# Kernel optimization log

Measured on AMD Instinct MI355X. Metric: run time of the kernel, lower is better.

## Reference

```python
import jax, jax.numpy as jnp
import numpy as np

B, C, H, W = 4, 256, 64, 64
EPS = 1e-6


def setup_inputs() -> dict:
    key = jax.random.key(0)
    ks = jax.random.split(key, 6)
    x = jax.random.normal(ks[0], (B, C, H, W), jnp.float32)
    gn_w = jnp.ones((1, C, 1, 1), jnp.float32)
    gn_b = jnp.zeros((1, C, 1, 1), jnp.float32)
    s = 1.0 / np.sqrt(C)
    w0 = jax.random.normal(ks[1], (C, C), jnp.float32) * s
    w1 = jax.random.normal(ks[2], (C, C), jnp.float32) * s
    w2 = jax.random.normal(ks[3], (C, C), jnp.float32) * s
    w3 = jax.random.normal(ks[4], (C, C), jnp.float32) * s
    b0 = jnp.zeros((C,), jnp.float32)
    b1 = jnp.zeros((C,), jnp.float32)
    b2 = jnp.zeros((C,), jnp.float32)
    b3 = jnp.zeros((C,), jnp.float32)
    return {"x": x, "gn_w": gn_w, "gn_b": gn_b,
            "w0": w0, "b0": b0, "w1": w1, "b1": b1,
            "w2": w2, "b2": b2, "w3": w3, "b3": b3}


def _nin(t, Wm, bv):
    # 1x1 conv as channel matmul: (B,C,H,W) x (C,D) -> (B,D,H,W)
    return jnp.einsum('bchw,cd->bdhw', t, Wm) + bv[None, :, None, None]


def reference(x, gn_w, gn_b, w0, b0, w1, b1, w2, b2, w3, b3):
    Bb, Cc, Hh, Ww = x.shape
    G = min(Cc // 4, 32)  # GroupLayerNorm2d groups
    # per-pixel group norm: normalize over channels within each group only
    xg = x.reshape(Bb, G, Cc // G, Hh, Ww)
    mean = xg.mean(axis=2, keepdims=True)
    var = xg.var(axis=2, keepdims=True)
    hn = ((xg - mean) / jnp.sqrt(var + EPS)).reshape(Bb, Cc, Hh, Ww)
    hn = hn * gn_w + gn_b
    q = _nin(hn, w0, b0)
    k = _nin(hn, w1, b1)
    v = _nin(hn, w2, b2)
    # full (B,H,W,H,W) scores; mask is causal along W only (key col j > query col w)
    scores = jnp.einsum('bchw,bcij->bhwij', q, k) * (float(Cc) ** -0.5)
    causal = jnp.triu(jnp.ones((Ww, Ww), bool), k=1)  # (W_query, W_key)
    scores = jnp.where(causal[None, None, :, None, :], -jnp.inf, scores)
    attn = jax.nn.softmax(scores.reshape(Bb, Hh, Ww, Hh * Ww), axis=-1)
    attn = attn.reshape(Bb, Hh, Ww, Hh, Ww)
    h = jnp.einsum('bhwij,bcij->bchw', attn, v)
    return x + _nin(h, w3, b3)  # skip_rescale=False
```

## Files before the change

### kernel.cpp

```cpp
#include <hip/hip_runtime.h>
#include <math.h>

#define LOG2E 1.4426950408889634f

typedef __attribute__((ext_vector_type(8))) __bf16 bf16x8_t;
typedef __attribute__((ext_vector_type(8))) short short8_t;
typedef __attribute__((ext_vector_type(4))) short short4_t;
typedef __attribute__((ext_vector_type(4))) float f32x4;

static __device__ __forceinline__ short f2bf(float f){
    unsigned u = __builtin_bit_cast(unsigned, f);
    unsigned r = (u + 0x7fffu + ((u >> 16) & 1u)) >> 16;
    return (short)r;
}
static __device__ __forceinline__ float bf2f(short s){
    return __builtin_bit_cast(float, (unsigned)((unsigned short)s) << 16);
}

static __device__ __forceinline__ f32x4 mfma16(short8_t a, short8_t b, f32x4 c){
    return __builtin_amdgcn_mfma_f32_16x16x32_bf16(
        __builtin_bit_cast(bf16x8_t, a), __builtin_bit_cast(bf16x8_t, b), c, 0, 0, 0);
}

static __device__ __forceinline__ float swz16(float v){
    return __builtin_bit_cast(float,
        __builtin_amdgcn_ds_swizzle(__builtin_bit_cast(int, v), 0x401F));
}
static __device__ __forceinline__ float bperm32(int addr, float v){
    return __builtin_bit_cast(float,
        __builtin_amdgcn_ds_bpermute(addr, __builtin_bit_cast(int, v)));
}

__global__ __launch_bounds__(256) void prep_w(const float* __restrict__ w0,
    const float* __restrict__ w1, const float* __restrict__ w2,
    const float* __restrict__ w3, short* __restrict__ wT)
{
    __shared__ float T[64 * 65];
    const int mat = blockIdx.x >> 4, tile = blockIdx.x & 15;
    const int c0 = (tile >> 2) * 64, d0 = (tile & 3) * 64;
    const float* src = mat == 0 ? w0 : mat == 1 ? w1 : mat == 2 ? w2 : w3;
    const int t = threadIdx.x;
    #pragma unroll
    for (int i = 0; i < 4; i++){
        int r = (t >> 4) + i * 16, c4 = (t & 15) * 4;
        f32x4 v = *(const f32x4*)(src + (size_t)(c0 + r) * 256 + d0 + c4);
        #pragma unroll
        for (int j = 0; j < 4; j++) T[r * 65 + c4 + j] = v[j];
    }
    __syncthreads();
    int drow = t >> 2, cb = (t & 3) * 16;
    short tmp[16];
    #pragma unroll
    for (int j = 0; j < 16; j++) tmp[j] = f2bf(T[(cb + j) * 65 + drow]);
    short* dst = wT + (size_t)mat * 65536 + (size_t)(d0 + drow) * 256 + c0 + cb;
    *(short8_t*)dst = *(short8_t*)tmp;
    *(short8_t*)(dst + 8) = *(short8_t*)(tmp + 8);
}

__global__ __launch_bounds__(256) void gn_kernel(const float* __restrict__ x,
    const float* __restrict__ gnw, const float* __restrict__ gnb,
    short* __restrict__ hn)
{
    int flat = blockIdx.x * 256 + threadIdx.x;
    int n = flat & 4095, g = (flat >> 12) & 31, b = flat >> 17;
    const float* xp = x + (size_t)(b * 256 + g * 8) * 4096 + n;
    float v[8], s = 0.f, s2 = 0.f;
    #pragma unroll
    for (int k = 0; k < 8; k++){ float t = xp[(size_t)k * 4096]; v[k] = t; s += t; s2 += t * t; }
    float mean = s * 0.125f;
    float var  = s2 * 0.125f - mean * mean;
    float inv  = rsqrtf(var + 1e-6f);
    int h = n >> 6, w = n & 63, m = w * 64 + h;
    short o[8];
    #pragma unroll
    for (int k = 0; k < 8; k++)
        o[k] = f2bf((v[k] - mean) * inv * gnw[g * 8 + k] + gnb[g * 8 + k]);
    *(short8_t*)(hn + (size_t)(b * 4096 + m) * 256 + g * 8) = *(short8_t*)o;
}

__global__ __launch_bounds__(256) void qkv_gemm(const short* __restrict__ hn,
    const short* __restrict__ wT, const float* __restrict__ bq,
    const float* __restrict__ bk, const float* __restrict__ bv,
    short* __restrict__ Q, short* __restrict__ Kf, short* __restrict__ Vf)
{
    __shared__ short As[64 * 72];
    __shared__ short Bs[64 * 72];
    __shared__ float CT[64 * 65];

    const int tid = threadIdx.x;
    const int m0 = blockIdx.x * 64;
    const int by = blockIdx.y;
    const int mat = by >> 2;
    const int d0 = (by & 3) * 64;
    const short* w = wT + mat * 65536;
    const float* bias = mat == 0 ? bq : mat == 1 ? bk : bv;

    const int wv = tid >> 6, lane = tid & 63;
    const int wrow = (wv >> 1) * 32, wcol = (wv & 1) * 32;
    const int lrow = lane & 15, lq = lane >> 4;

    f32x4 acc[2][2] = {};

    for (int k0 = 0; k0 < 256; k0 += 64){
        __syncthreads();
        #pragma unroll
        for (int i = 0; i < 2; i++){
            int idx = tid + i * 256, r = idx >> 3, c = (idx & 7) * 8;
            *(short8_t*)&As[r * 72 + c] = *(const short8_t*)(hn + (size_t)(m0 + r) * 256 + k0 + c);
            *(short8_t*)&Bs[r * 72 + c] = *(const short8_t*)(w  + (size_t)(d0 + r) * 256 + k0 + c);
        }
        __syncthreads();
        #pragma unroll
        for (int kk = 0; kk < 2; kk++){
            int off = kk * 32 + lq * 8;
            short8_t a0  = *(short8_t*)&As[(wrow + lrow) * 72 + off];
            short8_t a1  = *(short8_t*)&As[(wrow + 16 + lrow) * 72 + off];
            short8_t b0v = *(short8_t*)&Bs[(wcol + lrow) * 72 + off];
            short8_t b1v = *(short8_t*)&Bs[(wcol + 16 + lrow) * 72 + off];
            acc[0][0] = mfma16(a0, b0v, acc[0][0]);
            acc[0][1] = mfma16(a0, b1v, acc[0][1]);
            acc[1][0] = mfma16(a1, b0v, acc[1][0]);
            acc[1][1] = mfma16(a1, b1v, acc[1][1]);
        }
    }

    const int b = m0 >> 12, kb64 = (m0 & 4095) >> 6;

    if (mat == 0){
        #pragma unroll
        for (int i = 0; i < 2; i++)
          #pragma unroll
          for (int j = 0; j < 2; j++)
            #pragma unroll
            for (int r = 0; r < 4; r++){
                int row = wrow + i * 16 + lq * 4 + r;
                int col = wcol + j * 16 + lrow;
                Q[(size_t)(m0 + row) * 256 + d0 + col] = f2bf((acc[i][j][r] + bias[d0 + col]) * 0.0625f);
            }
    } else if (mat == 1){
        #pragma unroll
        for (int i = 0; i < 2; i++)
          #pragma unroll
          for (int j = 0; j < 2; j++)
            #pragma unroll
            for (int r = 0; r < 4; r++){
                int row = wrow + i * 16 + lq * 4 + r;
                int col = wcol + j * 16 + lrow;
                CT[row * 65 + col] = acc[i][j][r] + bias[d0 + col];
            }
        __syncthreads();
        int key = tid >> 2, c16 = (tid & 3) * 16;
        int kc = key >> 4, l15 = key & 15;
        #pragma unroll
        for (int half = 0; half < 2; half++){
            int ch0 = c16 + half * 8;
            int ks = (d0 + ch0) >> 5, lqf = (ch0 & 31) >> 3;
            short tmp[8];
            #pragma unroll
            for (int j = 0; j < 8; j++) tmp[j] = f2bf(CT[key * 65 + ch0 + j]);
            size_t base = ((((size_t)(b * 64 + kb64)) * 4 + kc) * 8 + ks) * 512 + (lqf * 16 + l15) * 8;
            *(short8_t*)(Kf + base) = *(short8_t*)tmp;
        }
    } else {
        #pragma unroll
        for (int i = 0; i < 2; i++)
          #pragma unroll
          for (int j = 0; j < 2; j++)
            #pragma unroll
            for (int r = 0; r < 4; r++){
                int row = wrow + i * 16 + lq * 4 + r;
                int col = wcol + j * 16 + lrow;
                CT[col * 65 + row] = acc[i][j][r] + bias[d0 + col];
            }
        __syncthreads();
        const int kbd = kb64 >> 1, parity = kb64 & 1;
        const int cht_l = tid >> 6, lane_s = tid & 63;
        const int l15s = lane_s & 15, lg4s = lane_s >> 4;
        const int cht = (d0 >> 4) + cht_l;
        #pragma unroll
        for (int kc = 0; kc < 4; kc++){
            short tmp[4];
            #pragma unroll
            for (int j = 0; j < 4; j++)
                tmp[j] = f2bf(CT[(cht_l * 16 + l15s) * 65 + kc * 16 + lg4s * 4 + j]);
            size_t base = (size_t)b * 1048576 + (size_t)kbd * 32768 + kc * 8192
                        + cht * 512 + lane_s * 8 + parity * 4;
            *(short4_t*)(Vf + base) = *(short4_t*)tmp;
        }
    }
}

__global__ __launch_bounds__(256, 2) void attn_kernel(const short* __restrict__ Q,
    const short* __restrict__ Kf, const short* __restrict__ Vf,
    short* __restrict__ hb)
{
    __shared__ float mls[4][16][2];
    __shared__ short LOs[4][16][264];

    const int tid = threadIdx.x, lane = tid & 63, kc = tid >> 6;
    const int l15 = lane & 15, lg4 = lane >> 4;
    const int a32 = ((lane ^ 32) << 2);

    const int id = blockIdx.x;
    const int qd = id >> 8, c = id & 255;
    const int w6 = c >> 2, hh = (c >> 1) & 1, rg = c & 1;
    const int b  = qd;
    const int w  = (qd & 1) ? 63 - w6 : w6;
    const int q0 = w * 64 + hh * 32 + rg * 16;

    const short* Kb = Kf + (size_t)b * 1048576 + kc * 4096 + lane * 8;
    const short* Vb = Vf + (size_t)b * 1048576 + kc * 8192 + lane * 8;

    short8_t qf[8];
    {
        const short* qp = Q + ((size_t)b * 4096 + q0 + l15) * 256;
        #pragma unroll
        for (int ks = 0; ks < 8; ks++)
            qf[ks] = *(const short8_t*)(qp + ks * 32 + lg4 * 8);
    }

    f32x4 oacc[16] = {};
    float m_run = -1e30f, l_run = 0.f;

    short8_t kcur[8], knext[8];
    #pragma unroll
    for (int ks = 0; ks < 8; ks++)
        kcur[ks] = *(const short8_t*)(Kb + ks * 512);

    for (int kb = 0; kb <= w; kb += 2){
        const bool has_odd = (kb + 1 <= w);
        if (has_odd){
            const short* kit = Kb + (size_t)(kb + 1) * 16384;
            #pragma unroll
            for (int ks = 0; ks < 8; ks++)
                knext[ks] = *(const short8_t*)(kit + ks * 512);
        }
        f32x4 st = {};
        #pragma unroll
        for (int ks = 0; ks < 8; ks++) st = mfma16(kcur[ks], qf[ks], st);

        if (kb + 2 <= w){
            const short* kit = Kb + (size_t)(kb + 2) * 16384;
            #pragma unroll
            for (int ks = 0; ks < 8; ks++)
                kcur[ks] = *(const short8_t*)(kit + ks * 512);
        }

        f32x4 st2 = { -1e30f, -1e30f, -1e30f, -1e30f };
        if (has_odd){
            f32x4 z = {};
            #pragma unroll
            for (int ks = 0; ks < 8; ks++) z = mfma16(knext[ks], qf[ks], z);
            st2 = z;
        }

        float tmax = fmaxf(fmaxf(fmaxf(st[0], st[1]), fmaxf(st[2], st[3])),
                           fmaxf(fmaxf(st2[0], st2[1]), fmaxf(st2[2], st2[3])));
        tmax = fmaxf(tmax, swz16(tmax));
        tmax = fmaxf(tmax, bperm32(a32, tmax));
        float m_new = fmaxf(m_run, tmax);
        float alpha = exp2f((m_run - m_new) * LOG2E);
        m_run = m_new;

        f32x4 p_e, p_o;
        #pragma unroll
        for (int r = 0; r < 4; r++){
            p_e[r] = exp2f((st[r]  - m_new) * LOG2E);
            p_o[r] = exp2f((st2[r] - m_new) * LOG2E);
        }
        float tsum = ((p_e[0] + p_e[1]) + (p_e[2] + p_e[3]))
                   + ((p_o[0] + p_o[1]) + (p_o[2] + p_o[3]));
        tsum += swz16(tsum);
        tsum += bperm32(a32, tsum);
        l_run = l_run * alpha + tsum;

        short pb[8];
        #pragma unroll
        for (int r = 0; r < 4; r++){ pb[r] = f2bf(p_e[r]); pb[4 + r] = f2bf(p_o[r]); }
        short8_t pbf = *(short8_t*)pb;

        const short* vit = Vb + (size_t)(kb >> 1) * 32768;
        #pragma unroll
        for (int cht = 0; cht < 16; cht++){
            short8_t vfr = *(const short8_t*)(vit + cht * 512);
            f32x4 t = oacc[cht];
            #pragma unroll
            for (int r = 0; r < 4; r++) t[r] *= alpha;
            oacc[cht] = mfma16(vfr, pbf, t);
        }
    }

    if (lg4 == 0){ mls[kc][l15][0] = m_run; mls[kc][l15][1] = l_run; }
    __syncthreads();
    float m0v = mls[0][l15][0], m1v = mls[1][l15][0], m2v = mls[2][l15][0], m3v = mls[3][l15][0];
    float mstar = fmaxf(fmaxf(m0v, m1v), fmaxf(m2v, m3v));
    float Lsum = mls[0][l15][1] * exp2f((m0v - mstar) * LOG2E)
               + mls[1][l15][1] * exp2f((m1v - mstar) * LOG2E)
               + mls[2][l15][1] * exp2f((m2v - mstar) * LOG2E)
               + mls[3][l15][1] * exp2f((m3v - mstar) * LOG2E);
    float sc = exp2f((m_run - mstar) * LOG2E);
    #pragma unroll
    for (int cht = 0; cht < 16; cht++){
        short t4[4];
        #pragma unroll
        for (int r = 0; r < 4; r++) t4[r] = f2bf(oacc[cht][r] * sc);
        *(short4_t*)&LOs[kc][l15][cht * 16 + lg4 * 4] = *(short4_t*)t4;
    }
    __syncthreads();
    {
        const int ch0 = kc * 64 + lg4 * 16;
        float inv = 1.f / Lsum;
        short tmp[16];
        #pragma unroll
        for (int c8 = 0; c8 < 2; c8++){
            short8_t a0 = *(const short8_t*)&LOs[0][l15][ch0 + c8 * 8];
            short8_t a1 = *(const short8_t*)&LOs[1][l15][ch0 + c8 * 8];
            short8_t a2 = *(const short8_t*)&LOs[2][l15][ch0 + c8 * 8];
            short8_t a3 = *(const short8_t*)&LOs[3][l15][ch0 + c8 * 8];
            #pragma unroll
            for (int j = 0; j < 8; j++){
                float s = (bf2f(a0[j]) + bf2f(a1[j])) + (bf2f(a2[j]) + bf2f(a3[j]));
                tmp[c8 * 8 + j] = f2bf(s * inv);
            }
        }
        const int h = hh * 32 + rg * 16 + l15;
        short* dst = hb + ((size_t)b * 4096 + h * 64 + w) * 256 + ch0;
        *(short8_t*)dst = *(short8_t*)tmp;
        *(short8_t*)(dst + 8) = *(short8_t*)(tmp + 8);
    }
}

__global__ __launch_bounds__(256) void final_gemm(const short* __restrict__ hbuf,
    const short* __restrict__ wT3, const float* __restrict__ b3,
    const float* __restrict__ x, float* __restrict__ out)
{
    __shared__ short As[64 * 72];
    __shared__ short Bs[64 * 72];
    __shared__ float CT[64 * 65];

    const int tid = threadIdx.x;
    const int m0 = blockIdx.x * 64;
    const int d0 = blockIdx.y * 64;
    const int wv = tid >> 6, lane = tid & 63;
    const int wrow = (wv >> 1) * 32, wcol = (wv & 1) * 32;
    const int lrow = lane & 15, lq = lane >> 4;

    f32x4 acc[2][2] = {};
    for (int k0 = 0; k0 < 256; k0 += 64){
        __syncthreads();
        #pragma unroll
        for (int i = 0; i < 2; i++){
            int idx = tid + i * 256, r = idx >> 3, c = (idx & 7) * 8;
            *(short8_t*)&As[r * 72 + c] = *(const short8_t*)(hbuf + (size_t)(m0 + r) * 256 + k0 + c);
            *(short8_t*)&Bs[r * 72 + c] = *(const short8_t*)(wT3 + (size_t)(d0 + r) * 256 + k0 + c);
        }
        __syncthreads();
        #pragma unroll
        for (int kk = 0; kk < 2; kk++){
            int off = kk * 32 + lq * 8;
            short8_t a0  = *(short8_t*)&As[(wrow + lrow) * 72 + off];
            short8_t a1  = *(short8_t*)&As[(wrow + 16 + lrow) * 72 + off];
            short8_t b0v = *(short8_t*)&Bs[(wcol + lrow) * 72 + off];
            short8_t b1v = *(short8_t*)&Bs[(wcol + 16 + lrow) * 72 + off];
            acc[0][0] = mfma16(a0, b0v, acc[0][0]);
            acc[0][1] = mfma16(a0, b1v, acc[0][1]);
            acc[1][0] = mfma16(a1, b0v, acc[1][0]);
            acc[1][1] = mfma16(a1, b1v, acc[1][1]);
        }
    }
    #pragma unroll
    for (int i = 0; i < 2; i++)
      #pragma unroll
      for (int j = 0; j < 2; j++)
        #pragma unroll
        for (int r = 0; r < 4; r++){
            int row = wrow + i * 16 + lq * 4 + r;
            int col = wcol + j * 16 + lrow;
            CT[col * 65 + row] = acc[i][j][r] + b3[d0 + col];
        }
    __syncthreads();
    int b = m0 >> 12, n0 = m0 & 4095, hrow = n0 >> 6;
    int dr = tid >> 2, wc = (tid & 3) * 16;
    size_t base = ((size_t)(b * 256 + d0 + dr) * 64 + hrow) * 64 + wc;
    const f32x4* xp = (const f32x4*)(x + base);
    f32x4* op = (f32x4*)(out + base);
    #pragma unroll
    for (int q = 0; q < 4; q++){
        f32x4 xv = xp[q], o;
        #pragma unroll
        for (int j = 0; j < 4; j++) o[j] = xv[j] + CT[dr * 65 + wc + q * 4 + j];
        op[q] = o;
    }
}

extern "C" void kernel_launch(void* const* d_in, const int* in_sizes, int n_in,
                              void* d_out, int out_size, void* d_ws, size_t ws_size,
                              hipStream_t stream)
{
    const float* x   = (const float*)d_in[0];
    const float* gnw = (const float*)d_in[1];
    const float* gnb = (const float*)d_in[2];
    const float* w0  = (const float*)d_in[3];
    const float* b0  = (const float*)d_in[4];
    const float* w1  = (const float*)d_in[5];
    const float* b1  = (const float*)d_in[6];
    const float* w2  = (const float*)d_in[7];
    const float* b2  = (const float*)d_in[8];
    const float* w3  = (const float*)d_in[9];
    const float* b3  = (const float*)d_in[10];
    float* out = (float*)d_out;

    char* ws = (char*)d_ws;
    short* wT  = (short*)(ws);
    short* hn  = (short*)(ws + 524288);
    short* Qb  = (short*)(ws + 8912896);
    short* Kfb = (short*)(ws + 17301504);
    short* Vfb = (short*)(ws + 25690112);
    short* hb  = (short*)(ws + 34078720);

    prep_w   <<<64, 256, 0, stream>>>(w0, w1, w2, w3, wT);
    gn_kernel<<<2048, 256, 0, stream>>>(x, gnw, gnb, hn);
    qkv_gemm <<<dim3(256, 12), 256, 0, stream>>>(hn, wT, b0, b1, b2, Qb, Kfb, Vfb);
    attn_kernel<<<1024, 256, 0, stream>>>(Qb, Kfb, Vfb, hb);
    final_gemm<<<dim3(256, 4), 256, 0, stream>>>(hb, wT + 3 * 65536, b3, x, out);
}
```

Baseline: 210.6 us.

## Fuse weight prep with groupnorm, restructure attention softmax with lazy rescale

Merges the weight-transpose and group-norm kernels into one launch to save a kernel launch. In the attention kernel it raises occupancy to 3 waves per SIMD, remaps block ids so each batch/half lands on one XCD for K/V cache locality, and uses a single K buffer. It switches to a lazy online-softmax rescale that only rescales the accumulator when the max grows by more than a threshold, and defers the row-sum reduction to the end. It also adds s_setprio around MFMA bursts and nontemporal Q loads. Risks include register spills at higher occupancy and bf16 overflow of unnormalized probabilities up to exp(5).

```diff
diff --git a/kernel.cpp b/kernel.cpp
--- a/kernel.cpp
+++ b/kernel.cpp
@@ -31,51 +31,50 @@
         __builtin_amdgcn_ds_bpermute(addr, __builtin_bit_cast(int, v)));
 }
 
-__global__ __launch_bounds__(256) void prep_w(const float* __restrict__ w0,
+__global__ __launch_bounds__(256) void prep_gn(const float* __restrict__ w0,
     const float* __restrict__ w1, const float* __restrict__ w2,
-    const float* __restrict__ w3, short* __restrict__ wT)
+    const float* __restrict__ w3, short* __restrict__ wT,
+    const float* __restrict__ x, const float* __restrict__ gnw,
+    const float* __restrict__ gnb, short* __restrict__ hn)
 {
     __shared__ float T[64 * 65];
-    const int mat = blockIdx.x >> 4, tile = blockIdx.x & 15;
-    const int c0 = (tile >> 2) * 64, d0 = (tile & 3) * 64;
-    const float* src = mat == 0 ? w0 : mat == 1 ? w1 : mat == 2 ? w2 : w3;
-    const int t = threadIdx.x;
-    #pragma unroll
-    for (int i = 0; i < 4; i++){
-        int r = (t >> 4) + i * 16, c4 = (t & 15) * 4;
-        f32x4 v = *(const f32x4*)(src + (size_t)(c0 + r) * 256 + d0 + c4);
-        #pragma unroll
-        for (int j = 0; j < 4; j++) T[r * 65 + c4 + j] = v[j];
-    }
-    __syncthreads();
-    int drow = t >> 2, cb = (t & 3) * 16;
-    short tmp[16];
-    #pragma unroll
-    for (int j = 0; j < 16; j++) tmp[j] = f2bf(T[(cb + j) * 65 + drow]);
-    short* dst = wT + (size_t)mat * 65536 + (size_t)(d0 + drow) * 256 + c0 + cb;
-    *(short8_t*)dst = *(short8_t*)tmp;
-    *(short8_t*)(dst + 8) = *(short8_t*)(tmp + 8);
-}
-
-__global__ __launch_bounds__(256) void gn_kernel(const float* __restrict__ x,
-    const float* __restrict__ gnw, const float* __restrict__ gnb,
-    short* __restrict__ hn)
-{
-    int flat = blockIdx.x * 256 + threadIdx.x;
-    int n = flat & 4095, g = (flat >> 12) & 31, b = flat >> 17;
-    const float* xp = x + (size_t)(b * 256 + g * 8) * 4096 + n;
-    float v[8], s = 0.f, s2 = 0.f;
-    #pragma unroll
-    for (int k = 0; k < 8; k++){ float t = xp[(size_t)k * 4096]; v[k] = t; s += t; s2 += t * t; }
-    float mean = s * 0.125f;
-    float var  = s2 * 0.125f - mean * mean;
-    float inv  = rsqrtf(var + 1e-6f);
-    int h = n >> 6, w = n & 63, m = w * 64 + h;
-    short o[8];
-    #pragma unroll
-    for (int k = 0; k < 8; k++)
-        o[k] = f2bf((v[k] - mean) * inv * gnw[g * 8 + k] + gnb[g * 8 + k]);
-    *(short8_t*)(hn + (size_t)(b * 4096 + m) * 256 + g * 8) = *(short8_t*)o;
+    if (blockIdx.x < 64){
+        const int mat = blockIdx.x >> 4, tile = blockIdx.x & 15;
+        const int c0 = (tile >> 2) * 64, d0 = (tile & 3) * 64;
+        const float* src = mat == 0 ? w0 : mat == 1 ? w1 : mat == 2 ? w2 : w3;
+        const int t = threadIdx.x;
+        #pragma unroll
+        for (int i = 0; i < 4; i++){
+            int r = (t >> 4) + i * 16, c4 = (t & 15) * 4;
+            f32x4 v = *(const f32x4*)(src + (size_t)(c0 + r) * 256 + d0 + c4);
+            #pragma unroll
+            for (int j = 0; j < 4; j++) T[r * 65 + c4 + j] = v[j];
+        }
+        __syncthreads();
+        int drow = t >> 2, cb = (t & 3) * 16;
+        short tmp[16];
+        #pragma unroll
+        for (int j = 0; j < 16; j++) tmp[j] = f2bf(T[(cb + j) * 65 + drow]);
+        short* dst = wT + (size_t)mat * 65536 + (size_t)(d0 + drow) * 256 + c0 + cb;
+        *(short8_t*)dst = *(short8_t*)tmp;
+        *(short8_t*)(dst + 8) = *(short8_t*)(tmp + 8);
+    } else {
+        int flat = (blockIdx.x - 64) * 256 + threadIdx.x;
+        int n = flat & 4095, g = (flat >> 12) & 31, b = flat >> 17;
+        const float* xp = x + (size_t)(b * 256 + g * 8) * 4096 + n;
+        float v[8], s = 0.f, s2 = 0.f;
+        #pragma unroll
+        for (int k = 0; k < 8; k++){ float t = xp[(size_t)k * 4096]; v[k] = t; s += t; s2 += t * t; }
+        float mean = s * 0.125f;
+        float var  = s2 * 0.125f - mean * mean;
+        float inv  = rsqrtf(var + 1e-6f);
+        int h = n >> 6, w = n & 63, m = w * 64 + h;
+        short o[8];
+        #pragma unroll
+        for (int k = 0; k < 8; k++)
+            o[k] = f2bf((v[k] - mean) * inv * gnw[g * 8 + k] + gnb[g * 8 + k]);
+        *(short8_t*)(hn + (size_t)(b * 4096 + m) * 256 + g * 8) = *(short8_t*)o;
+    }
 }
 
 __global__ __launch_bounds__(256) void qkv_gemm(const short* __restrict__ hn,
@@ -190,23 +189,26 @@
     }
 }
 
-__global__ __launch_bounds__(256, 2) void attn_kernel(const short* __restrict__ Q,
+__global__ __launch_bounds__(256, 3) void attn_kernel(const short* __restrict__ Q,
     const short* __restrict__ Kf, const short* __restrict__ Vf,
     short* __restrict__ hb)
 {
+    __shared__ short LOs[4][16][264];
     __shared__ float mls[4][16][2];
-    __shared__ short LOs[4][16][264];
 
     const int tid = threadIdx.x, lane = tid & 63, kc = tid >> 6;
     const int l15 = lane & 15, lg4 = lane >> 4;
     const int a32 = ((lane ^ 32) << 2);
 
-    const int id = blockIdx.x;
-    const int qd = id >> 8, c = id & 255;
-    const int w6 = c >> 2, hh = (c >> 1) & 1, rg = c & 1;
-    const int b  = qd;
-    const int w  = (qd & 1) ? 63 - w6 : w6;
-    const int q0 = w * 64 + hh * 32 + rg * 16;
+    const int id  = blockIdx.x;
+    const int xcd = id & 7;
+    const int b   = xcd >> 1;
+    const int hh  = xcd & 1;
+    const int r_  = id >> 3;
+    const int rg  = r_ & 1;
+    const int t_  = (r_ >> 1) & 31;
+    const int w   = (r_ & 64) ? 63 - t_ : t_;
+    const int q0  = w * 64 + hh * 32 + rg * 16;
 
     const short* Kb = Kf + (size_t)b * 1048576 + kc * 4096 + lane * 8;
     const short* Vb = Vf + (size_t)b * 1048576 + kc * 8192 + lane * 8;
@@ -216,81 +218,100 @@
         const short* qp = Q + ((size_t)b * 4096 + q0 + l15) * 256;
         #pragma unroll
         for (int ks = 0; ks < 8; ks++)
-            qf[ks] = *(const short8_t*)(qp + ks * 32 + lg4 * 8);
+            qf[ks] = __builtin_nontemporal_load((const short8_t*)(qp + ks * 32 + lg4 * 8));
     }
 
     f32x4 oacc[16] = {};
-    float m_run = -1e30f, l_run = 0.f;
-
-    short8_t kcur[8], knext[8];
+    float m0 = -1e30f, l0 = 0.f;
+
+    short8_t kf[8];
     #pragma unroll
-    for (int ks = 0; ks < 8; ks++)
-        kcur[ks] = *(const short8_t*)(Kb + ks * 512);
+    for (int ks = 0; ks < 8; ks++) kf[ks] = *(const short8_t*)(Kb + ks * 512);
 
     for (int kb = 0; kb <= w; kb += 2){
         const bool has_odd = (kb + 1 <= w);
+
+        f32x4 stA = {};
+        __builtin_amdgcn_s_setprio(1);
+        #pragma unroll
+        for (int ks = 0; ks < 8; ks++) stA = mfma16(kf[ks], qf[ks], stA);
+        __builtin_amdgcn_s_setprio(0);
         if (has_odd){
-            const short* kit = Kb + (size_t)(kb + 1) * 16384;
-            #pragma unroll
-            for (int ks = 0; ks < 8; ks++)
-                knext[ks] = *(const short8_t*)(kit + ks * 512);
-        }
-        f32x4 st = {};
-        #pragma unroll
-        for (int ks = 0; ks < 8; ks++) st = mfma16(kcur[ks], qf[ks], st);
-
-        if (kb + 2 <= w){
-            const short* kit = Kb + (size_t)(kb + 2) * 16384;
-            #pragma unroll
-            for (int ks = 0; ks < 8; ks++)
-                kcur[ks] = *(const short8_t*)(kit + ks * 512);
-        }
-
-        f32x4 st2 = { -1e30f, -1e30f, -1e30f, -1e30f };
+            const short* ka = Kb + (size_t)(kb + 1) * 16384;
+            #pragma unroll
+            for (int ks = 0; ks < 8; ks++) kf[ks] = *(const short8_t*)(ka + ks * 512);
+        }
+
+        f32x4 pA;
+        {
+            float tl = fmaxf(fmaxf(stA[0], stA[1]), fmaxf(stA[2], stA[3]));
+            if (!__all(tl <= m0 + 5.f)){
+                float tm = fmaxf(tl, swz16(tl)); tm = fmaxf(tm, bperm32(a32, tm));
+                float mn = fmaxf(m0, tm);
+                float al = exp2f((m0 - mn) * LOG2E);
+                l0 *= al;
+                #pragma unroll
+                for (int i = 0; i < 16; i++){
+                    #pragma unroll
+                    for (int r = 0; r < 4; r++) oacc[i][r] *= al;
+                }
+                m0 = mn;
+            }
+            #pragma unroll
+            for (int r = 0; r < 4; r++) pA[r] = exp2f((stA[r] - m0) * LOG2E);
+            l0 += (pA[0] + pA[1]) + (pA[2] + pA[3]);
+        }
+
+        f32x4 pB = {0.f, 0.f, 0.f, 0.f};
         if (has_odd){
-            f32x4 z = {};
-            #pragma unroll
-            for (int ks = 0; ks < 8; ks++) z = mfma16(knext[ks], qf[ks], z);
-            st2 = z;
-        }
-
-        float tmax = fmaxf(fmaxf(fmaxf(st[0], st[1]), fmaxf(st[2], st[3])),
-                           fmaxf(fmaxf(st2[0], st2[1]), fmaxf(st2[2], st2[3])));
-        tmax = fmaxf(tmax, swz16(tmax));
-        tmax = fmaxf(tmax, bperm32(a32, tmax));
-        float m_new = fmaxf(m_run, tmax);
-        float alpha = exp2f((m_run - m_new) * LOG2E);
-        m_run = m_new;
-
-        f32x4 p_e, p_o;
-        #pragma unroll
-        for (int r = 0; r < 4; r++){
-            p_e[r] = exp2f((st[r]  - m_new) * LOG2E);
-            p_o[r] = exp2f((st2[r] - m_new) * LOG2E);
-        }
-        float tsum = ((p_e[0] + p_e[1]) + (p_e[2] + p_e[3]))
-                   + ((p_o[0] + p_o[1]) + (p_o[2] + p_o[3]));
-        tsum += swz16(tsum);
-        tsum += bperm32(a32, tsum);
-        l_run = l_run * alpha + tsum;
-
-        short pb[8];
-        #pragma unroll
-        for (int r = 0; r < 4; r++){ pb[r] = f2bf(p_e[r]); pb[4 + r] = f2bf(p_o[r]); }
-        short8_t pbf = *(short8_t*)pb;
+            f32x4 stB = {};
+            __builtin_amdgcn_s_setprio(1);
+            #pragma unroll
+            for (int ks = 0; ks < 8; ks++) stB = mfma16(kf[ks], qf[ks], stB);
+            __builtin_amdgcn_s_setprio(0);
+            if (kb + 2 <= w){
+                const short* ka = Kb + (size_t)(kb + 2) * 16384;
+                #pragma unroll
+                for (int ks = 0; ks < 8; ks++) kf[ks] = *(const short8_t*)(ka + ks * 512);
+            }
+            float tl = fmaxf(fmaxf(stB[0], stB[1]), fmaxf(stB[2], stB[3]));
+            if (!__all(tl <= m0 + 5.f)){
+                float tm = fmaxf(tl, swz16(tl)); tm = fmaxf(tm, bperm32(a32, tm));
+                float mn = fmaxf(m0, tm);
+                float al = exp2f((m0 - mn) * LOG2E);
+                l0 *= al;
+                #pragma unroll
+                for (int i = 0; i < 16; i++){
+                    #pragma unroll
+                    for (int r = 0; r < 4; r++) oacc[i][r] *= al;
+                }
+                #pragma unroll
+                for (int r = 0; r < 4; r++) pA[r] *= al;
+                m0 = mn;
+            }
+            #pragma unroll
+            for (int r = 0; r < 4; r++) pB[r] = exp2f((stB[r] - m0) * LOG2E);
+            l0 += (pB[0] + pB[1]) + (pB[2] + pB[3]);
+        }
+
+        short pk[8];
+        #pragma unroll
+        for (int r = 0; r < 4; r++){ pk[r] = f2bf(pA[r]); pk[4 + r] = f2bf(pB[r]); }
+        short8_t pbf = *(short8_t*)pk;
 
         const short* vit = Vb + (size_t)(kb >> 1) * 32768;
+        __builtin_amdgcn_s_setprio(1);
         #pragma unroll
         for (int cht = 0; cht < 16; cht++){
             short8_t vfr = *(const short8_t*)(vit + cht * 512);
-            f32x4 t = oacc[cht];
-            #pragma unroll
-            for (int r = 0; r < 4; r++) t[r] *= alpha;
-            oacc[cht] = mfma16(vfr, pbf, t);
-        }
-    }
-
-    if (lg4 == 0){ mls[kc][l15][0] = m_run; mls[kc][l15][1] = l_run; }
+            oacc[cht] = mfma16(vfr, pbf, oacc[cht]);
+        }
+        __builtin_amdgcn_s_setprio(0);
+    }
+
+    float l0t = l0 + swz16(l0); l0t += bperm32(a32, l0t);
+
+    if (lg4 == 0){ mls[kc][l15][0] = m0; mls[kc][l15][1] = l0t; }
     __syncthreads();
     float m0v = mls[0][l15][0], m1v = mls[1][l15][0], m2v = mls[2][l15][0], m3v = mls[3][l15][0];
     float mstar = fmaxf(fmaxf(m0v, m1v), fmaxf(m2v, m3v));
@@ -298,7 +319,7 @@
                + mls[1][l15][1] * exp2f((m1v - mstar) * LOG2E)
                + mls[2][l15][1] * exp2f((m2v - mstar) * LOG2E)
                + mls[3][l15][1] * exp2f((m3v - mstar) * LOG2E);
-    float sc = exp2f((m_run - mstar) * LOG2E);
+    float sc = exp2f((m0 - mstar) * LOG2E);
     #pragma unroll
     for (int cht = 0; cht < 16; cht++){
         short t4[4];
@@ -418,8 +439,7 @@
     short* Vfb = (short*)(ws + 25690112);
     short* hb  = (short*)(ws + 34078720);
 
-    prep_w   <<<64, 256, 0, stream>>>(w0, w1, w2, w3, wT);
-    gn_kernel<<<2048, 256, 0, stream>>>(x, gnw, gnb, hn);
+    prep_gn  <<<2112, 256, 0, stream>>>(w0, w1, w2, w3, wT, x, gnw, gnb, hn);
     qkv_gemm <<<dim3(256, 12), 256, 0, stream>>>(hn, wT, b0, b1, b2, Qb, Kfb, Vfb);
     attn_kernel<<<1024, 256, 0, stream>>>(Qb, Kfb, Vfb, hb);
     final_gemm<<<dim3(256, 4), 256, 0, stream>>>(hb, wT + 3 * 65536, b3, x, out);
```

Result: faster. 201.4 us (-4.4%).
